# Kernel optimization log

Hardware: AMD Instinct MI355X
Metric: run time of the kernel (lower is better)

Reference implementation:

```python
import jax, jax.numpy as jnp
import numpy as np
from jax import lax

BS, CNT, W, P, E, K, L = 32, 128, 2048, 1024, 8, 25, 2


def setup_inputs() -> dict:
    key = jax.random.key(0)
    ks = jax.random.split(key, 12)
    s = lambda k, shape, scale: jax.random.normal(k, shape, dtype=jnp.float32) * scale
    return {
        "x": s(ks[0], (BS, CNT, W), 1.0),
        "conv_w": s(ks[1], (L, E, 1, K), 0.2),
        "conv_b": s(ks[2], (L, E), 0.02),
        "wq": s(ks[3], (L, P, W), 0.02),
        "bq": s(ks[4], (L, P), 0.02),
        "wk": s(ks[5], (L, P, W), 0.02),
        "bk": s(ks[6], (L, P), 0.02),
        "wv": s(ks[7], (L, P, W), 0.02),
        "bv": s(ks[8], (L, P), 0.02),
        "wo": s(ks[9], (L, W, P), 0.02),
        "bo": s(ks[10], (L, W), 0.02),
    }


def _moe(x, w, b):
    # x: [bs, cnt, W]; w: [E, 1, K]; b: [E]
    bs, cnt, d = x.shape
    xf = x.reshape(bs * cnt, 1, d)
    pad = K // 2
    y = lax.conv_general_dilated(
        xf, w, window_strides=(1,), padding=[(pad, pad)],
        dimension_numbers=("NCH", "OIH", "NCH"))  # [bs*cnt, E, W]
    y = y + b[None, :, None]
    return y.mean(axis=1).reshape(bs, cnt, d)


def _fe(x, wq, bq, wk, bk, wv, bv, wo, bo):
    # x: [bs, cnt, W]; projections to P, FFT-domain attention, back to W
    q = jnp.einsum("bcw,pw->bcp", x, wq) + bq
    k = jnp.einsum("bcw,pw->bcp", x, wk) + bk
    v = jnp.einsum("bcw,pw->bcp", x, wv) + bv
    q_fft = jnp.fft.fft(q, axis=-1)
    k_fft = jnp.fft.fft(k, axis=-1)
    v_fft = jnp.fft.fft(v, axis=-1)
    scale = jnp.sqrt(jnp.float32(P))
    weighted = (k_fft * jnp.conj(q_fft)) / scale * v_fft
    wv_real = jnp.fft.ifft(weighted, axis=-1).real.astype(x.dtype)
    return jnp.einsum("bcp,wp->bcw", wv_real, wo) + bo


def reference(x, conv_w, conv_b, wq, bq, wk, bk, wv, bv, wo, bo):
    for l in range(L):
        x = _moe(x, conv_w[l], conv_b[l])
        x = _fe(x, wq[l], bq[l], wk[l], bk[l], wv[l], bv[l], wo[l], bo[l])
    return x
```

## Files before the change

### kernel.cpp

```cpp
#include <hip/hip_runtime.h>
#include <hip/hip_bf16.h>

#define BSZ 32
#define CNTS 128
#define WD 2048
#define PD 1024
#define ED 8
#define KSZ 25
#define LN 2
#define MROWS (BSZ*CNTS)
#define QKVN (3*PD)
#define NWL (PD*WD)

typedef _Float16 f16;
typedef __attribute__((ext_vector_type(8))) _Float16 f16x8;
typedef __attribute__((ext_vector_type(4))) float f32x4;
typedef __attribute__((ext_vector_type(2))) float f32x2;

#define PI_F 3.14159265358979323846f

__global__ __launch_bounds__(256) void cvt_layer(
    const float* __restrict__ wq, const float* __restrict__ wk,
    const float* __restrict__ wv, const float* __restrict__ wo,
    f16* __restrict__ wqkv16, f16* __restrict__ wo16)
{
    const int i = (blockIdx.x * 256 + threadIdx.x) * 4;
    const float* src;
    f16* dst;
    if (i < 3*NWL) {
        dst = wqkv16 + i;
        src = (i < NWL) ? wq + i : (i < 2*NWL) ? wk + (i - NWL) : wv + (i - 2*NWL);
    } else {
        dst = wo16 + (i - 3*NWL);
        src = wo + (i - 3*NWL);
    }
    const float4 v = *(const float4*)src;
    f16 o[4];
    o[0] = (f16)v.x; o[1] = (f16)v.y; o[2] = (f16)v.z; o[3] = (f16)v.w;
    *(ushort4*)dst = *(const ushort4*)o;
}

template<typename IT>
__global__ __launch_bounds__(256) void conv_moe(
    const IT* __restrict__ xin,
    const float* __restrict__ cw,
    const float* __restrict__ cb,
    f16* __restrict__ xo)
{
    __shared__ float srow[WD];
    __shared__ float swb[KSZ];
    __shared__ float sbb;
    const int tid = threadIdx.x;
    const size_t row = blockIdx.x;
    if (tid < KSZ) {
        float s = 0.f;
        for (int e = 0; e < ED; ++e) s += cw[e*KSZ + tid];
        swb[tid] = s * (1.f/ED);
    }
    if (tid == 32) {
        float s = 0.f;
        for (int e = 0; e < ED; ++e) s += cb[e];
        sbb = s * (1.f/ED);
    }
    const IT* xr = xin + row*WD;
    if constexpr (sizeof(IT) == 2) {
        const f16x8 v = *(const f16x8*)(xr + tid*8);
        #pragma unroll
        for (int j = 0; j < 8; ++j) srow[tid*8 + j] = (float)v[j];
    } else {
        const float4 v0 = *(const float4*)(xr + tid*8);
        const float4 v1 = *(const float4*)(xr + tid*8 + 4);
        srow[tid*8+0] = v0.x; srow[tid*8+1] = v0.y; srow[tid*8+2] = v0.z; srow[tid*8+3] = v0.w;
        srow[tid*8+4] = v1.x; srow[tid*8+5] = v1.y; srow[tid*8+6] = v1.z; srow[tid*8+7] = v1.w;
    }
    __syncthreads();
    const float bb = sbb;
    float w[32];
    #pragma unroll
    for (int k = 0; k < 32; ++k) {
        const int idx = tid*8 + k - (KSZ/2);
        w[k] = (idx >= 0 && idx < WD) ? srow[idx] : 0.f;
    }
    f16 o[8];
    #pragma unroll
    for (int j = 0; j < 8; ++j) {
        float acc = bb;
        #pragma unroll
        for (int k = 0; k < KSZ; ++k) acc = fmaf(w[j+k], swb[k], acc);
        o[j] = (f16)acc;
    }
    *(f16x8*)(xo + row*WD + tid*8) = *(const f16x8*)o;
}

__global__ __launch_bounds__(512, 2) void gemm192(
    const f16* __restrict__ A,
    const f16* __restrict__ B,
    const float* __restrict__ c0, const float* __restrict__ c1, const float* __restrict__ c2,
    f16* __restrict__ out,
    const int K, const int N)
{
    __shared__ __align__(16) f16 sA[2][2][128*64];
    __shared__ __align__(16) f16 sB[2][3][64*64];

    const int tid  = threadIdx.x;
    const int lane = tid & 63;
    const int wave = tid >> 6;
    const int wr   = wave >> 2;
    const int wc   = wave & 3;
    const int quad = lane >> 4;
    const int r16  = lane & 15;
    const int xrA  = r16 & 7;

    const int orig = blockIdx.x;
    const int xcd  = orig & 7;
    const int loc  = orig >> 3;
    const int mt   = (xcd >> 1) * 4 + (loc & 3);
    const int nt   = (xcd & 1) * 8 + (loc >> 2);
    const int m0   = mt * 256;
    const int n0   = nt * 192;

    f32x4 acc[8][3] = {};
    f16x8 bf[3][2];
    f16x8 aX0, aX1, aX2, aX3, aY0, aY1, aY2, aY3, aZ0, aZ1, aZ2, aZ3;

    int soffA[2];
    #pragma unroll
    for (int t = 0; t < 2; ++t) {
        const int s = tid + 512*t;
        const int row = s >> 3;
        soffA[t] = row * K + (((s & 7) ^ (row & 7)) * 8);
    }
    int soffB;
    {
        const int row = tid >> 3;
        soffB = row * K + (((tid & 7) ^ (row & 7)) * 8);
    }

    int bPiece[3], bBase[3], bXor[3];
    #pragma unroll
    for (int j = 0; j < 3; ++j) {
        const int rb = wc*48 + j*16 + r16;
        bPiece[j] = rb >> 6;
        bBase[j]  = (rb & 63) << 3;
        bXor[j]   = rb & 7;
    }

    const f16* Abase[2] = { A + (size_t)m0 * K, A + (size_t)(m0 + 128) * K };
    const f16* Bp[3]    = { B + (size_t)n0 * K, B + (size_t)(n0 + 64) * K,
                            B + (size_t)(n0 + 128) * K };

    #define STAGE_A(BUF, HALF, GOFF)                                              \
      { _Pragma("unroll") for (int t = 0; t < 2; ++t) {                           \
          __builtin_amdgcn_global_load_lds(                                       \
            (const __attribute__((address_space(1))) unsigned int*)(Abase[HALF] + soffA[t] + (GOFF)), \
            (__attribute__((address_space(3))) unsigned int*)&sA[BUF][HALF][(tid + 512*t)*8], \
            16, 0, 0); } }

    #define STAGE_B(BUF, PIECE, GOFF)                                             \
      { __builtin_amdgcn_global_load_lds(                                         \
          (const __attribute__((address_space(1))) unsigned int*)(Bp[PIECE] + soffB + (GOFF)), \
          (__attribute__((address_space(3))) unsigned int*)&sB[BUF][PIECE][tid*8], \
          16, 0, 0); }

    #define LDA(BUF, ROW, C) \
      (*(const f16x8*)&sA[BUF][wr][ (((ROW) << 3) + ((C) ^ xrA)) * 8 ])

    #define LDB(BUF, J, C) \
      (*(const f16x8*)&sB[BUF][bPiece[J]][ (bBase[J] + ((C) ^ bXor[J])) * 8 ])

    #define READ_BF(BUF)                                                          \
      { _Pragma("unroll") for (int j = 0; j < 3; ++j) {                           \
          bf[j][0] = LDB(BUF, j, quad);                                           \
          bf[j][1] = LDB(BUF, j, 4 + quad);                                       \
        } }

    #define READ_A(BUF, Q, D0, D1, D2, D3)                                        \
      D0 = LDA(BUF, (2*(Q))*16   + r16, quad);                                    \
      D1 = LDA(BUF, (2*(Q))*16   + r16, 4 + quad);                                \
      D2 = LDA(BUF, (2*(Q)+1)*16 + r16, quad);                                    \
      D3 = LDA(BUF, (2*(Q)+1)*16 + r16, 4 + quad);

    #define MFMA_Q(Q, D0, D1, D2, D3)                                             \
      __builtin_amdgcn_s_setprio(1);                                              \
      { _Pragma("unroll") for (int jj = 0; jj < 3; ++jj) {                        \
          acc[2*(Q)][jj]   = __builtin_amdgcn_mfma_f32_16x16x32_f16(D0, bf[jj][0], acc[2*(Q)][jj],   0,0,0); \
          acc[2*(Q)+1][jj] = __builtin_amdgcn_mfma_f32_16x16x32_f16(D2, bf[jj][0], acc[2*(Q)+1][jj], 0,0,0); \
        } }                                                                       \
      { _Pragma("unroll") for (int jj = 0; jj < 3; ++jj) {                        \
          acc[2*(Q)][jj]   = __builtin_amdgcn_mfma_f32_16x16x32_f16(D1, bf[jj][1], acc[2*(Q)][jj],   0,0,0); \
          acc[2*(Q)+1][jj] = __builtin_amdgcn_mfma_f32_16x16x32_f16(D3, bf[jj][1], acc[2*(Q)+1][jj], 0,0,0); \
        } }                                                                       \
      __builtin_amdgcn_s_setprio(0);

    #define LGKM(n) asm volatile("s_waitcnt lgkmcnt(" #n ")" ::: "memory");       \
                    __builtin_amdgcn_sched_barrier(0);
    #define VMC(n)  asm volatile("s_waitcnt vmcnt(" #n ")" ::: "memory");
    #define BAR()   __builtin_amdgcn_s_barrier();

    STAGE_B(0, 0, 0); STAGE_B(0, 1, 0); STAGE_B(0, 2, 0);
    STAGE_A(0, 0, 0); STAGE_A(0, 1, 0);
    STAGE_B(1, 0, 64); STAGE_B(1, 1, 64); STAGE_B(1, 2, 64);
    VMC(3)
    BAR()

    const int NIT = K >> 7;
    for (int it = 0; it < NIT; ++it) {
        const bool kl = (it == NIT - 1);
        const int kb1 = (2*it + 1) * 64;
        const int kb2 = kb1 + 64;
        const int kb3 = kb1 + 128;

        STAGE_A(1, 0, kb1);
        READ_BF(0)
        READ_A(0, 0, aX0, aX1, aX2, aX3)
        LGKM(0)
        MFMA_Q(0, aX0, aX1, aX2, aX3)
        BAR()
        STAGE_A(1, 1, kb1);
        READ_A(0, 1, aY0, aY1, aY2, aY3)
        READ_A(0, 2, aZ0, aZ1, aZ2, aZ3)
        LGKM(4)
        MFMA_Q(1, aY0, aY1, aY2, aY3)
        if (!kl) { STAGE_B(0, 0, kb2); STAGE_B(0, 1, kb2); }
        READ_A(0, 3, aX0, aX1, aX2, aX3)
        LGKM(4)
        MFMA_Q(2, aZ0, aZ1, aZ2, aZ3)
        if (!kl) { STAGE_B(0, 2, kb2); }
        LGKM(0)
        MFMA_Q(3, aX0, aX1, aX2, aX3)
        if (!kl) { VMC(3) } else { VMC(0) }
        BAR()

        if (!kl) STAGE_A(0, 0, kb2);
        READ_BF(1)
        READ_A(1, 0, aX0, aX1, aX2, aX3)
        LGKM(0)
        MFMA_Q(0, aX0, aX1, aX2, aX3)
        BAR()
        if (!kl) STAGE_A(0, 1, kb2);
        READ_A(1, 1, aY0, aY1, aY2, aY3)
        READ_A(1, 2, aZ0, aZ1, aZ2, aZ3)
        LGKM(4)
        MFMA_Q(1, aY0, aY1, aY2, aY3)
        if (!kl) { STAGE_B(1, 0, kb3); STAGE_B(1, 1, kb3); }
        READ_A(1, 3, aX0, aX1, aX2, aX3)
        LGKM(4)
        MFMA_Q(2, aZ0, aZ1, aZ2, aZ3)
        if (!kl) { STAGE_B(1, 2, kb3); }
        LGKM(0)
        MFMA_Q(3, aX0, aX1, aX2, aX3)
        if (!kl) { VMC(3) }
        BAR()
    }

    #pragma unroll
    for (int j = 0; j < 3; ++j) {
        const int col = n0 + wc*48 + j*16 + r16;
        const float bv = (col < 1024) ? c0[col] : (col < 2048) ? c1[col-1024] : c2[col-2048];
        #pragma unroll
        for (int mi = 0; mi < 8; ++mi) {
            #pragma unroll
            for (int r = 0; r < 4; ++r) {
                const int rowg = m0 + wr*128 + mi*16 + quad*4 + r;
                out[(size_t)rowg*N + col] = (f16)(acc[mi][j][r] + bv);
            }
        }
    }

    #undef STAGE_A
    #undef STAGE_B
    #undef LDA
    #undef LDB
    #undef READ_BF
    #undef READ_A
    #undef MFMA_Q
    #undef LGKM
    #undef VMC
    #undef BAR
}

template<typename OT>
__global__ __launch_bounds__(512, 2) void gemmOP(
    const f16* __restrict__ A,
    const f16* __restrict__ B,
    const float* __restrict__ c0, const float* __restrict__ c1,
    OT* __restrict__ out,
    const int K, const int N)
{
    __shared__ __align__(16) f16 sA[2][2][128*64];
    __shared__ __align__(16) f16 sB[2][2][64*64];

    const int tid  = threadIdx.x;
    const int lane = tid & 63;
    const int wave = tid >> 6;
    const int wr   = wave >> 2;
    const int wc   = wave & 3;
    const int quad = lane >> 4;
    const int r16  = lane & 15;
    const int xrA  = r16 & 7;

    const int orig = blockIdx.x;
    const int xcd  = orig & 7;
    const int loc  = orig >> 3;
    const int mt   = (xcd >> 1) * 4 + (loc & 3);
    const int nt   = (xcd & 1) * 8 + (loc >> 2);
    const int m0   = mt * 256;
    const int n0   = nt * 128;

    f32x4 acc[8][2] = {};
    f16x8 bf[2][2];
    f16x8 aX0, aX1, aX2, aX3, aY0, aY1, aY2, aY3, aZ0, aZ1, aZ2, aZ3;

    int soffA[2];
    #pragma unroll
    for (int t = 0; t < 2; ++t) {
        const int s = tid + 512*t;
        const int row = s >> 3;
        soffA[t] = row * K + (((s & 7) ^ (row & 7)) * 8);
    }
    int soffB;
    {
        const int row = tid >> 3;
        soffB = row * K + (((tid & 7) ^ (row & 7)) * 8);
    }

    int bPiece[2], bBase[2], bXor[2];
    #pragma unroll
    for (int j = 0; j < 2; ++j) {
        const int rb = wc*32 + j*16 + r16;
        bPiece[j] = rb >> 6;
        bBase[j]  = (rb & 63) << 3;
        bXor[j]   = rb & 7;
    }

    const f16* Abase[2] = { A + (size_t)m0 * K, A + (size_t)(m0 + 128) * K };
    const f16* Bp[2]    = { B + (size_t)n0 * K, B + (size_t)(n0 + 64) * K };

    #define STAGE_A(BUF, HALF, GOFF)                                              \
      { _Pragma("unroll") for (int t = 0; t < 2; ++t) {                           \
          __builtin_amdgcn_global_load_lds(                                       \
            (const __attribute__((address_space(1))) unsigned int*)(Abase[HALF] + soffA[t] + (GOFF)), \
            (__attribute__((address_space(3))) unsigned int*)&sA[BUF][HALF][(tid + 512*t)*8], \
            16, 0, 0); } }

    #define STAGE_B(BUF, PIECE, GOFF)                                             \
      { __builtin_amdgcn_global_load_lds(                                         \
          (const __attribute__((address_space(1))) unsigned int*)(Bp[PIECE] + soffB + (GOFF)), \
          (__attribute__((address_space(3))) unsigned int*)&sB[BUF][PIECE][tid*8], \
          16, 0, 0); }

    #define LDA(BUF, ROW, C) \
      (*(const f16x8*)&sA[BUF][wr][ (((ROW) << 3) + ((C) ^ xrA)) * 8 ])

    #define LDB(BUF, J, C) \
      (*(const f16x8*)&sB[BUF][bPiece[J]][ (bBase[J] + ((C) ^ bXor[J])) * 8 ])

    #define READ_BF(BUF)                                                          \
      { _Pragma("unroll") for (int j = 0; j < 2; ++j) {                           \
          bf[j][0] = LDB(BUF, j, quad);                                           \
          bf[j][1] = LDB(BUF, j, 4 + quad);                                       \
        } }

    #define READ_A(BUF, Q, D0, D1, D2, D3)                                        \
      D0 = LDA(BUF, (2*(Q))*16   + r16, quad);                                    \
      D1 = LDA(BUF, (2*(Q))*16   + r16, 4 + quad);                                \
      D2 = LDA(BUF, (2*(Q)+1)*16 + r16, quad);                                    \
      D3 = LDA(BUF, (2*(Q)+1)*16 + r16, 4 + quad);

    #define MFMA_Q(Q, D0, D1, D2, D3)                                             \
      __builtin_amdgcn_s_setprio(1);                                              \
      { _Pragma("unroll") for (int jj = 0; jj < 2; ++jj) {                        \
          acc[2*(Q)][jj]   = __builtin_amdgcn_mfma_f32_16x16x32_f16(D0, bf[jj][0], acc[2*(Q)][jj],   0,0,0); \
          acc[2*(Q)+1][jj] = __builtin_amdgcn_mfma_f32_16x16x32_f16(D2, bf[jj][0], acc[2*(Q)+1][jj], 0,0,0); \
        } }                                                                       \
      { _Pragma("unroll") for (int jj = 0; jj < 2; ++jj) {                        \
          acc[2*(Q)][jj]   = __builtin_amdgcn_mfma_f32_16x16x32_f16(D1, bf[jj][1], acc[2*(Q)][jj],   0,0,0); \
          acc[2*(Q)+1][jj] = __builtin_amdgcn_mfma_f32_16x16x32_f16(D3, bf[jj][1], acc[2*(Q)+1][jj], 0,0,0); \
        } }                                                                       \
      __builtin_amdgcn_s_setprio(0);

    #define LGKM(n) asm volatile("s_waitcnt lgkmcnt(" #n ")" ::: "memory");       \
                    __builtin_amdgcn_sched_barrier(0);
    #define VMC(n)  asm volatile("s_waitcnt vmcnt(" #n ")" ::: "memory");
    #define BAR()   __builtin_amdgcn_s_barrier();

    STAGE_B(0, 0, 0); STAGE_B(0, 1, 0);
    STAGE_A(0, 0, 0); STAGE_A(0, 1, 0);
    STAGE_B(1, 0, 64); STAGE_B(1, 1, 64);
    VMC(2)
    BAR()

    const int NIT = K >> 7;
    for (int it = 0; it < NIT; ++it) {
        const bool kl = (it == NIT - 1);
        const int kb1 = (2*it + 1) * 64;
        const int kb2 = kb1 + 64;
        const int kb3 = kb1 + 128;

        STAGE_A(1, 0, kb1);
        READ_BF(0)
        READ_A(0, 0, aX0, aX1, aX2, aX3)
        LGKM(0)
        MFMA_Q(0, aX0, aX1, aX2, aX3)
        BAR()
        STAGE_A(1, 1, kb1);
        READ_A(0, 1, aY0, aY1, aY2, aY3)
        READ_A(0, 2, aZ0, aZ1, aZ2, aZ3)
        LGKM(4)
        MFMA_Q(1, aY0, aY1, aY2, aY3)
        if (!kl) { STAGE_B(0, 0, kb2); }
        READ_A(0, 3, aX0, aX1, aX2, aX3)
        LGKM(4)
        MFMA_Q(2, aZ0, aZ1, aZ2, aZ3)
        if (!kl) { STAGE_B(0, 1, kb2); }
        LGKM(0)
        MFMA_Q(3, aX0, aX1, aX2, aX3)
        if (!kl) { VMC(2) } else { VMC(0) }
        BAR()

        if (!kl) STAGE_A(0, 0, kb2);
        READ_BF(1)
        READ_A(1, 0, aX0, aX1, aX2, aX3)
        LGKM(0)
        MFMA_Q(0, aX0, aX1, aX2, aX3)
        BAR()
        if (!kl) STAGE_A(0, 1, kb2);
        READ_A(1, 1, aY0, aY1, aY2, aY3)
        READ_A(1, 2, aZ0, aZ1, aZ2, aZ3)
        LGKM(4)
        MFMA_Q(1, aY0, aY1, aY2, aY3)
        if (!kl) { STAGE_B(1, 0, kb3); }
        READ_A(1, 3, aX0, aX1, aX2, aX3)
        LGKM(4)
        MFMA_Q(2, aZ0, aZ1, aZ2, aZ3)
        if (!kl) { STAGE_B(1, 1, kb3); }
        LGKM(0)
        MFMA_Q(3, aX0, aX1, aX2, aX3)
        if (!kl) { VMC(2) }
        BAR()
    }

    #pragma unroll
    for (int j = 0; j < 2; ++j) {
        const int col = n0 + wc*32 + j*16 + r16;
        const float bv = (col < 1024) ? c0[col] : c1[col-1024];
        #pragma unroll
        for (int mi = 0; mi < 8; ++mi) {
            #pragma unroll
            for (int r = 0; r < 4; ++r) {
                const int rowg = m0 + wr*128 + mi*16 + quad*4 + r;
                out[(size_t)rowg*N + col] = (OT)(acc[mi][j][r] + bv);
            }
        }
    }

    #undef STAGE_A
    #undef STAGE_B
    #undef LDA
    #undef LDB
    #undef READ_BF
    #undef READ_A
    #undef MFMA_Q
    #undef LGKM
    #undef VMC
    #undef BAR
}

__device__ __forceinline__ f32x2 cmul2(const f32x2 a, const float wc, const float ws) {
    f32x2 r; r.x = a.x*wc - a.y*ws; r.y = a.y*wc + a.x*ws; return r;
}

#define IZ(c,i) ((c)*65 + ((i) ^ ((((i) >> 4) & 3) << 2)))
#define WSYNC() { asm volatile("s_waitcnt lgkmcnt(0)" ::: "memory"); \
                  __builtin_amdgcn_sched_barrier(0); }

__global__ __launch_bounds__(256) void fft_attn_wave(
    const f16* __restrict__ qkv, f16* __restrict__ outg)
{
    __shared__ f32x2 ZZ[4][2][16*65];
    const int tid = threadIdx.x;
    const int w   = tid >> 6;
    const int l   = tid & 63;
    const int t   = l & 15;
    const int cg  = l >> 4;
    f32x2* Z1 = &ZZ[w][0][0];
    f32x2* Z2 = &ZZ[w][1][0];
    f16*   sc = (f16*)Z1;

    const size_t rp = (size_t)blockIdx.x*4 + w;
    const f16* r1 = qkv + (2*rp)*QKVN;
    const f16* r2 = r1 + QKVN;

    float bwc[16], bws[16];
    {
        const float th = -2.f*PI_F*(float)l*(1.f/1024.f);
        bwc[0]=1.f; bws[0]=0.f;
        __sincosf(th,     &bws[1], &bwc[1]);
        __sincosf(2.f*th, &bws[2], &bwc[2]);
        __sincosf(4.f*th, &bws[4], &bwc[4]);
        __sincosf(8.f*th, &bws[8], &bwc[8]);
        bwc[3]=bwc[1]*bwc[2]-bws[1]*bws[2]; bws[3]=bws[1]*bwc[2]+bwc[1]*bws[2];
        bwc[5]=bwc[1]*bwc[4]-bws[1]*bws[4]; bws[5]=bws[1]*bwc[4]+bwc[1]*bws[4];
        bwc[6]=bwc[2]*bwc[4]-bws[2]*bws[4]; bws[6]=bws[2]*bwc[4]+bwc[2]*bws[4];
        bwc[7]=bwc[3]*bwc[4]-bws[3]*bws[4]; bws[7]=bws[3]*bwc[4]+bwc[3]*bws[4];
        #pragma unroll
        for (int k = 9; k < 16; ++k) {
            bwc[k]=bwc[k-8]*bwc[8]-bws[k-8]*bws[8];
            bws[k]=bws[k-8]*bwc[8]+bwc[k-8]*bws[8];
        }
    }
    float c0s, c0c, c1s, c1c;
    __sincosf(-2.f*PI_F*(float)t*(1.f/64.f), &c0s, &c0c);
    __sincosf(-2.f*PI_F*(float)(t>>2)*(1.f/16.f), &c1s, &c1c);

    const float W16C[10] = {1.f, 0.92387953f, 0.70710678f, 0.38268343f, 0.f,
                            0.f, -0.70710678f, 0.f, 0.f, -0.92387953f};
    const float W16S[10] = {0.f, -0.38268343f, -0.70710678f, -0.92387953f, -1.f,
                            0.f, -0.70710678f, 0.f, 0.f, 0.38268343f};

    f32x2 v[16], V1[16], V2[16];

    auto run_fft = [&]() {
        f32x2 C[4][4];
        #pragma unroll
        for (int jj = 0; jj < 4; ++jj) {
            const f32x2 a = v[jj], b = v[jj+4], c = v[jj+8], d = v[jj+12];
            f32x2 t0, t1, t2, t3;
            t0.x=a.x+c.x; t0.y=a.y+c.y; t1.x=a.x-c.x; t1.y=a.y-c.y;
            t2.x=b.x+d.x; t2.y=b.y+d.y; t3.x=b.x-d.x; t3.y=b.y-d.y;
            f32x2 B0, B1, B2, B3;
            B0.x=t0.x+t2.x; B0.y=t0.y+t2.y;
            B1.x=t1.x+t3.y; B1.y=t1.y-t3.x;
            B2.x=t0.x-t2.x; B2.y=t0.y-t2.y;
            B3.x=t1.x-t3.y; B3.y=t1.y+t3.x;
            C[0][jj] = B0;
            C[1][jj] = cmul2(B1, W16C[jj],   W16S[jj]);
            C[2][jj] = cmul2(B2, W16C[2*jj], W16S[2*jj]);
            C[3][jj] = cmul2(B3, W16C[3*jj], W16S[3*jj]);
        }
        f32x2 g[16];
        #pragma unroll
        for (int q = 0; q < 4; ++q) {
            const f32x2 c0 = C[q][0], c1 = C[q][1], c2 = C[q][2], c3 = C[q][3];
            f32x2 e0, o0, e1, o1;
            e0.x=c0.x+c2.x; e0.y=c0.y+c2.y; o0.x=c1.x+c3.x; o0.y=c1.y+c3.y;
            e1.x=c0.x-c2.x; e1.y=c0.y-c2.y; o1.x=c1.x-c3.x; o1.y=c1.y-c3.y;
            g[q].x    = e0.x+o0.x; g[q].y    = e0.y+o0.y;
            g[q+4].x  = e1.x+o1.y; g[q+4].y  = e1.y-o1.x;
            g[q+8].x  = e0.x-o0.x; g[q+8].y  = e0.y-o0.y;
            g[q+12].x = e1.x-o1.y; g[q+12].y = e1.y+o1.x;
        }
        WSYNC()
        #pragma unroll
        for (int k = 0; k < 16; ++k)
            Z1[IZ(k, l)] = cmul2(g[k], bwc[k], bws[k]);
        WSYNC()
        #pragma unroll
        for (int pass = 0; pass < 4; ++pass) {
            const int c = cg + 4*pass;
            const f32x2 a = Z1[IZ(c, t)],     b = Z1[IZ(c, t+16)];
            const f32x2 cc = Z1[IZ(c, t+32)], d = Z1[IZ(c, t+48)];
            const float apcx=a.x+cc.x, apcy=a.y+cc.y, amcx=a.x-cc.x, amcy=a.y-cc.y;
            const float bpdx=b.x+d.x,  bpdy=b.y+d.y,  bmdx=b.x-d.x,  bmdy=b.y-d.y;
            f32x2 y0; y0.x=apcx+bpdx; y0.y=apcy+bpdy;
            const float t1x=amcx+bmdy, t1y=amcy-bmdx;
            const float t2x=apcx-bpdx, t2y=apcy-bpdy;
            const float t3x=amcx-bmdy, t3y=amcy+bmdx;
            const float w2x=c0c*c0c-c0s*c0s, w2y=2.f*c0c*c0s;
            const float w3x=w2x*c0c-w2y*c0s, w3y=w2x*c0s+w2y*c0c;
            f32x2 y1; y1.x=c0c*t1x-c0s*t1y; y1.y=c0c*t1y+c0s*t1x;
            f32x2 y2; y2.x=w2x*t2x-w2y*t2y; y2.y=w2x*t2y+w2y*t2x;
            f32x2 y3; y3.x=w3x*t3x-w3y*t3y; y3.y=w3x*t3y+w3y*t3x;
            const int i0 = 4*t;
            Z2[IZ(c, i0)]   = y0; Z2[IZ(c, i0+1)] = y1;
            Z2[IZ(c, i0+2)] = y2; Z2[IZ(c, i0+3)] = y3;
        }
        WSYNC()
        #pragma unroll
        for (int pass = 0; pass < 4; ++pass) {
            const int c = cg + 4*pass;
            const f32x2 a = Z2[IZ(c, t)],     b = Z2[IZ(c, t+16)];
            const f32x2 cc = Z2[IZ(c, t+32)], d = Z2[IZ(c, t+48)];
            const float apcx=a.x+cc.x, apcy=a.y+cc.y, amcx=a.x-cc.x, amcy=a.y-cc.y;
            const float bpdx=b.x+d.x,  bpdy=b.y+d.y,  bmdx=b.x-d.x,  bmdy=b.y-d.y;
            f32x2 y0; y0.x=apcx+bpdx; y0.y=apcy+bpdy;
            const float t1x=amcx+bmdy, t1y=amcy-bmdx;
            const float t2x=apcx-bpdx, t2y=apcy-bpdy;
            const float t3x=amcx-bmdy, t3y=amcy+bmdx;
            const float w2x=c1c*c1c-c1s*c1s, w2y=2.f*c1c*c1s;
            const float w3x=w2x*c1c-w2y*c1s, w3y=w2x*c1s+w2y*c1c;
            f32x2 y1; y1.x=c1c*t1x-c1s*t1y; y1.y=c1c*t1y+c1s*t1x;
            f32x2 y2; y2.x=w2x*t2x-w2y*t2y; y2.y=w2x*t2y+w2y*t2x;
            f32x2 y3; y3.x=w3x*t3x-w3y*t3y; y3.y=w3x*t3y+w3y*t3x;
            const int i0 = (t & 3) + 16*(t >> 2);
            Z1[IZ(c, i0)]    = y0; Z1[IZ(c, i0+4)]  = y1;
            Z1[IZ(c, i0+8)]  = y2; Z1[IZ(c, i0+12)] = y3;
        }
        WSYNC()
        #pragma unroll
        for (int pass = 0; pass < 4; ++pass) {
            const int c = cg + 4*pass;
            const f32x2 a = Z1[IZ(c, t)],     b = Z1[IZ(c, t+16)];
            const f32x2 cc = Z1[IZ(c, t+32)], d = Z1[IZ(c, t+48)];
            const float apcx=a.x+cc.x, apcy=a.y+cc.y, amcx=a.x-cc.x, amcy=a.y-cc.y;
            const float bpdx=b.x+d.x,  bpdy=b.y+d.y,  bmdx=b.x-d.x,  bmdy=b.y-d.y;
            f32x2 y0; y0.x=apcx+bpdx; y0.y=apcy+bpdy;
            f32x2 y1; y1.x=amcx+bmdy; y1.y=amcy-bmdx;
            f32x2 y2; y2.x=apcx-bpdx; y2.y=apcy-bpdy;
            f32x2 y3; y3.x=amcx-bmdy; y3.y=amcy+bmdx;
            Z2[IZ(c, t)]    = y0; Z2[IZ(c, t+16)] = y1;
            Z2[IZ(c, t+32)] = y2; Z2[IZ(c, t+48)] = y3;
        }
        WSYNC()
    };

    auto stage2 = [&](const f16* a, const f16* b) {
        const f16x8 a0 = *(const f16x8*)(a + l*8);
        const f16x8 a1 = *(const f16x8*)(a + (l+64)*8);
        const f16x8 b0 = *(const f16x8*)(b + l*8);
        const f16x8 b1 = *(const f16x8*)(b + (l+64)*8);
        WSYNC()
        *(f16x8*)&sc[l*8]          = a0;
        *(f16x8*)&sc[(l+64)*8]     = a1;
        *(f16x8*)&sc[1024+l*8]     = b0;
        *(f16x8*)&sc[1024+(l+64)*8]= b1;
        WSYNC()
    };

    stage2(r1 + 2048, r2 + 2048);
    #pragma unroll
    for (int j = 0; j < 16; ++j) {
        v[j].x = (float)sc[l + 64*j];
        v[j].y = (float)sc[1024 + l + 64*j];
    }
    run_fft();
    #pragma unroll
    for (int j = 0; j < 16; ++j) {
        const int f = l + 64*j;
        const int gg = (PD - f) & (PD-1);
        const f32x2 z1 = Z2[IZ(f & 15, f >> 4)];
        const f32x2 z2 = Z2[IZ(gg & 15, gg >> 4)];
        V1[j].x = 0.5f*(z1.x + z2.x); V1[j].y = 0.5f*(z1.y - z2.y);
        V2[j].x = 0.5f*(z1.y + z2.y); V2[j].y = 0.5f*(z2.x - z1.x);
    }

    {
        const f16x8 a0 = *(const f16x8*)(r1 + l*8);
        const f16x8 a1 = *(const f16x8*)(r1 + (l+64)*8);
        const f16x8 a2 = *(const f16x8*)(r1 + (l+128)*8);
        const f16x8 a3 = *(const f16x8*)(r1 + (l+192)*8);
        WSYNC()
        *(f16x8*)&sc[l*8]        = a0;
        *(f16x8*)&sc[(l+64)*8]   = a1;
        *(f16x8*)&sc[(l+128)*8]  = a2;
        *(f16x8*)&sc[(l+192)*8]  = a3;
        WSYNC()
    }
    #pragma unroll
    for (int j = 0; j < 16; ++j) {
        v[j].x = (float)sc[l + 64*j];
        v[j].y = (float)sc[1024 + l + 64*j];
    }
    run_fft();
    #pragma unroll
    for (int j = 0; j < 16; ++j) {
        const int f = l + 64*j;
        const int gg = (PD - f) & (PD-1);
        const f32x2 z1 = Z2[IZ(f & 15, f >> 4)];
        const f32x2 z2 = Z2[IZ(gg & 15, gg >> 4)];
        const float Qr = 0.5f*(z1.x + z2.x), Qi = 0.5f*(z1.y - z2.y);
        const float Kr = 0.5f*(z1.y + z2.y), Ki = 0.5f*(z2.x - z1.x);
        const float Pr = (Kr*Qr + Ki*Qi) * (1.f/32.f);
        const float Pi = (Ki*Qr - Kr*Qi) * (1.f/32.f);
        const float sx = Pr*V1[j].x - Pi*V1[j].y;
        const float sy = -(Pr*V1[j].y + Pi*V1[j].x);
        V1[j].x = sx; V1[j].y = sy;
    }

    {
        const f16x8 a0 = *(const f16x8*)(r2 + l*8);
        const f16x8 a1 = *(const f16x8*)(r2 + (l+64)*8);
        const f16x8 a2 = *(const f16x8*)(r2 + (l+128)*8);
        const f16x8 a3 = *(const f16x8*)(r2 + (l+192)*8);
        WSYNC()
        *(f16x8*)&sc[l*8]        = a0;
        *(f16x8*)&sc[(l+64)*8]   = a1;
        *(f16x8*)&sc[(l+128)*8]  = a2;
        *(f16x8*)&sc[(l+192)*8]  = a3;
        WSYNC()
    }
    #pragma unroll
    for (int j = 0; j < 16; ++j) {
        v[j].x = (float)sc[l + 64*j];
        v[j].y = (float)sc[1024 + l + 64*j];
    }
    run_fft();
    #pragma unroll
    for (int j = 0; j < 16; ++j) {
        const int f = l + 64*j;
        const int gg = (PD - f) & (PD-1);
        const f32x2 z1 = Z2[IZ(f & 15, f >> 4)];
        const f32x2 z2 = Z2[IZ(gg & 15, gg >> 4)];
        const float Qr = 0.5f*(z1.x + z2.x), Qi = 0.5f*(z1.y - z2.y);
        const float Kr = 0.5f*(z1.y + z2.y), Ki = 0.5f*(z2.x - z1.x);
        const float Pr = (Kr*Qr + Ki*Qi) * (1.f/32.f);
        const float Pi = (Ki*Qr - Kr*Qi) * (1.f/32.f);
        const float sx = Pr*V2[j].x - Pi*V2[j].y;
        const float sy = -(Pr*V2[j].y + Pi*V2[j].x);
        V2[j].x = sx; V2[j].y = sy;
    }

    #pragma unroll
    for (int j = 0; j < 16; ++j) {
        v[j].x = V1[j].x - V2[j].y;
        v[j].y = V1[j].y + V2[j].x;
    }
    run_fft();

    #pragma unroll
    for (int j = 0; j < 16; ++j) {
        const int n = l + 64*j;
        const f32x2 z = Z2[IZ(n & 15, n >> 4)];
        sc[n]        = (f16)(z.x * (1.f/1024.f));
        sc[1024 + n] = (f16)(z.y * (1.f/1024.f));
    }
    WSYNC()
    f16* o1 = outg + (2*rp)*PD;
    f16* o2 = o1 + PD;
    *(f16x8*)(o1 + l*8)      = *(const f16x8*)&sc[l*8];
    *(f16x8*)(o1 + (l+64)*8) = *(const f16x8*)&sc[(l+64)*8];
    *(f16x8*)(o2 + l*8)      = *(const f16x8*)&sc[1024 + l*8];
    *(f16x8*)(o2 + (l+64)*8) = *(const f16x8*)&sc[1024 + (l+64)*8];
}

extern "C" void kernel_launch(void* const* d_in, const int* in_sizes, int n_in,
                              void* d_out, int out_size, void* d_ws, size_t ws_size,
                              hipStream_t stream)
{
    const float* x      = (const float*)d_in[0];
    const float* conv_w = (const float*)d_in[1];
    const float* conv_b = (const float*)d_in[2];
    const float* wq     = (const float*)d_in[3];
    const float* bq     = (const float*)d_in[4];
    const float* wk     = (const float*)d_in[5];
    const float* bk     = (const float*)d_in[6];
    const float* wv     = (const float*)d_in[7];
    const float* bv     = (const float*)d_in[8];
    const float* wo     = (const float*)d_in[9];
    const float* bo     = (const float*)d_in[10];

    char* ws = (char*)d_ws;
    const size_t MB = 1024*1024;
    f16*   wqkv16 = (f16*)(ws);
    f16*   wo16   = (f16*)(ws + 12*MB);
    f16*   qkvbuf = (f16*)(ws + 16*MB);
    f16*   xc16   = (f16*)(ws + 40*MB);
    f16*   xmid   = (f16*)(ws + 56*MB);
    f16*   wvr16  = xc16;

    for (int l = 0; l < LN; ++l) {
        cvt_layer<<<dim3(4*NWL/4/256), dim3(256), 0, stream>>>(
            wq + (size_t)l*NWL, wk + (size_t)l*NWL, wv + (size_t)l*NWL, wo + (size_t)l*NWL,
            wqkv16, wo16);

        if (l == 0)
            conv_moe<float><<<dim3(MROWS), dim3(256), 0, stream>>>(
                x, conv_w, conv_b, xc16);
        else
            conv_moe<f16><<<dim3(MROWS), dim3(256), 0, stream>>>(
                xmid, conv_w + (size_t)l*ED*KSZ, conv_b + (size_t)l*ED, xc16);

        gemm192<<<dim3((MROWS/256)*(QKVN/192)), dim3(512), 0, stream>>>(
            xc16, wqkv16,
            bq + (size_t)l*PD, bk + (size_t)l*PD, bv + (size_t)l*PD,
            qkvbuf, WD, QKVN);

        fft_attn_wave<<<dim3(MROWS/8), dim3(256), 0, stream>>>(qkvbuf, wvr16);

        if (l == LN-1)
            gemmOP<float><<<dim3((MROWS/256)*(WD/128)), dim3(512), 0, stream>>>(
                wvr16, wo16,
                bo + (size_t)l*WD, bo + (size_t)l*WD + PD,
                (float*)d_out, PD, WD);
        else
            gemmOP<f16><<<dim3((MROWS/256)*(WD/128)), dim3(512), 0, stream>>>(
                wvr16, wo16,
                bo + (size_t)l*WD, bo + (size_t)l*WD + PD,
                xmid, PD, WD);
    }
}
```

Baseline: 427.0 us.

## Fuse per-layer kernels into persistent megakernel with grid barriers

Replaces the five per-layer launches (weight conversion, conv, QKV GEMM, FFT attention, output GEMM) with one persistent 256-block kernel per layer. The phases are separated by atomic-counter grid barriers and reuse one shared memory buffer. The goal is to remove launch gaps and tail effects between the small kernels. In exchange it forces one block per CU with a fixed grid, which can hurt occupancy in the GEMM and FFT phases. It also relies on all 256 blocks being co-resident for the barriers to avoid deadlock.

```diff
diff --git a/kernel.cpp b/kernel.cpp
--- a/kernel.cpp
+++ b/kernel.cpp
@@ -19,88 +19,40 @@
 
 #define PI_F 3.14159265358979323846f
 
-__global__ __launch_bounds__(256) void cvt_layer(
-    const float* __restrict__ wq, const float* __restrict__ wk,
-    const float* __restrict__ wv, const float* __restrict__ wo,
-    f16* __restrict__ wqkv16, f16* __restrict__ wo16)
+__device__ unsigned g_cnt[8];
+
+__device__ __forceinline__ void grid_barrier(int b)
 {
-    const int i = (blockIdx.x * 256 + threadIdx.x) * 4;
-    const float* src;
-    f16* dst;
-    if (i < 3*NWL) {
-        dst = wqkv16 + i;
-        src = (i < NWL) ? wq + i : (i < 2*NWL) ? wk + (i - NWL) : wv + (i - 2*NWL);
-    } else {
-        dst = wo16 + (i - 3*NWL);
-        src = wo + (i - 3*NWL);
-    }
-    const float4 v = *(const float4*)src;
-    f16 o[4];
-    o[0] = (f16)v.x; o[1] = (f16)v.y; o[2] = (f16)v.z; o[3] = (f16)v.w;
-    *(ushort4*)dst = *(const ushort4*)o;
+    __syncthreads();
+    if (threadIdx.x == 0) {
+        __threadfence();
+        const unsigned old = __hip_atomic_fetch_add(&g_cnt[b], 1u,
+                                __ATOMIC_ACQ_REL, __HIP_MEMORY_SCOPE_AGENT);
+        const unsigned target = (old & ~255u) + 256u;
+        while (__hip_atomic_load(&g_cnt[b],
+                   __ATOMIC_ACQUIRE, __HIP_MEMORY_SCOPE_AGENT) < target)
+            __builtin_amdgcn_s_sleep(2);
+    }
+    __syncthreads();
 }
 
-template<typename IT>
-__global__ __launch_bounds__(256) void conv_moe(
-    const IT* __restrict__ xin,
-    const float* __restrict__ cw,
-    const float* __restrict__ cb,
-    f16* __restrict__ xo)
+__device__ __forceinline__ f32x2 cmul2(const f32x2 a, const float wc, const float ws) {
+    f32x2 r; r.x = a.x*wc - a.y*ws; r.y = a.y*wc + a.x*ws; return r;
+}
+
+#define IZ(c,i) ((c)*65 + ((i) ^ ((((i) >> 4) & 3) << 2)))
+#define WSYNC() { asm volatile("s_waitcnt lgkmcnt(0)" ::: "memory"); \
+                  __builtin_amdgcn_sched_barrier(0); }
+
+__device__ __forceinline__ void gemm192_phase(
+    char* smem,
+    const f16* __restrict__ A, const f16* __restrict__ B,
+    const float* __restrict__ c0, const float* __restrict__ c1, const float* __restrict__ c2,
+    f16* __restrict__ out)
 {
-    __shared__ float srow[WD];
-    __shared__ float swb[KSZ];
-    __shared__ float sbb;
-    const int tid = threadIdx.x;
-    const size_t row = blockIdx.x;
-    if (tid < KSZ) {
-        float s = 0.f;
-        for (int e = 0; e < ED; ++e) s += cw[e*KSZ + tid];
-        swb[tid] = s * (1.f/ED);
-    }
-    if (tid == 32) {
-        float s = 0.f;
-        for (int e = 0; e < ED; ++e) s += cb[e];
-        sbb = s * (1.f/ED);
-    }
-    const IT* xr = xin + row*WD;
-    if constexpr (sizeof(IT) == 2) {
-        const f16x8 v = *(const f16x8*)(xr + tid*8);
-        #pragma unroll
-        for (int j = 0; j < 8; ++j) srow[tid*8 + j] = (float)v[j];
-    } else {
-        const float4 v0 = *(const float4*)(xr + tid*8);
-        const float4 v1 = *(const float4*)(xr + tid*8 + 4);
-        srow[tid*8+0] = v0.x; srow[tid*8+1] = v0.y; srow[tid*8+2] = v0.z; srow[tid*8+3] = v0.w;
-        srow[tid*8+4] = v1.x; srow[tid*8+5] = v1.y; srow[tid*8+6] = v1.z; srow[tid*8+7] = v1.w;
-    }
-    __syncthreads();
-    const float bb = sbb;
-    float w[32];
-    #pragma unroll
-    for (int k = 0; k < 32; ++k) {
-        const int idx = tid*8 + k - (KSZ/2);
-        w[k] = (idx >= 0 && idx < WD) ? srow[idx] : 0.f;
-    }
-    f16 o[8];
-    #pragma unroll
-    for (int j = 0; j < 8; ++j) {
-        float acc = bb;
-        #pragma unroll
-        for (int k = 0; k < KSZ; ++k) acc = fmaf(w[j+k], swb[k], acc);
-        o[j] = (f16)acc;
-    }
-    *(f16x8*)(xo + row*WD + tid*8) = *(const f16x8*)o;
-}
-
-__global__ __launch_bounds__(512, 2) void gemm192(
-    const f16* __restrict__ A,
-    const f16* __restrict__ B,
-    const float* __restrict__ c0, const float* __restrict__ c1, const float* __restrict__ c2,
-    f16* __restrict__ out,
-    const int K, const int N)
-{
-    __shared__ __align__(16) f16 sA[2][2][128*64];
-    __shared__ __align__(16) f16 sB[2][3][64*64];
+    const int K = WD, N = QKVN;
+    f16* sAb = (f16*)smem;
+    f16* sBb = (f16*)(smem + 65536);
 
     const int tid  = threadIdx.x;
     const int lane = tid & 63;
@@ -149,24 +101,27 @@
     const f16* Bp[3]    = { B + (size_t)n0 * K, B + (size_t)(n0 + 64) * K,
                             B + (size_t)(n0 + 128) * K };
 
+    #define G1_SA(BUF,HALF) (sAb + ((BUF)*2 + (HALF)) * 8192)
+    #define G1_SB(BUF,PIECE) (sBb + ((BUF)*3 + (PIECE)) * 4096)
+
     #define STAGE_A(BUF, HALF, GOFF)                                              \
       { _Pragma("unroll") for (int t = 0; t < 2; ++t) {                           \
           __builtin_amdgcn_global_load_lds(                                       \
             (const __attribute__((address_space(1))) unsigned int*)(Abase[HALF] + soffA[t] + (GOFF)), \
-            (__attribute__((address_space(3))) unsigned int*)&sA[BUF][HALF][(tid + 512*t)*8], \
+            (__attribute__((address_space(3))) unsigned int*)(G1_SA(BUF,HALF) + (tid + 512*t)*8), \
             16, 0, 0); } }
 
     #define STAGE_B(BUF, PIECE, GOFF)                                             \
       { __builtin_amdgcn_global_load_lds(                                         \
           (const __attribute__((address_space(1))) unsigned int*)(Bp[PIECE] + soffB + (GOFF)), \
-          (__attribute__((address_space(3))) unsigned int*)&sB[BUF][PIECE][tid*8], \
+          (__attribute__((address_space(3))) unsigned int*)(G1_SB(BUF,PIECE) + tid*8), \
           16, 0, 0); }
 
     #define LDA(BUF, ROW, C) \
-      (*(const f16x8*)&sA[BUF][wr][ (((ROW) << 3) + ((C) ^ xrA)) * 8 ])
+      (*(const f16x8*)(G1_SA(BUF,wr) + ((((ROW) << 3) + ((C) ^ xrA)) * 8)))
 
     #define LDB(BUF, J, C) \
-      (*(const f16x8*)&sB[BUF][bPiece[J]][ (bBase[J] + ((C) ^ bXor[J])) * 8 ])
+      (*(const f16x8*)(G1_SB(BUF,bPiece[J]) + ((bBase[J] + ((C) ^ bXor[J])) * 8)))
 
     #define READ_BF(BUF)                                                          \
       { _Pragma("unroll") for (int j = 0; j < 3; ++j) {                           \
@@ -267,6 +222,8 @@
         }
     }
 
+    #undef G1_SA
+    #undef G1_SB
     #undef STAGE_A
     #undef STAGE_B
     #undef LDA
@@ -280,15 +237,15 @@
 }
 
 template<typename OT>
-__global__ __launch_bounds__(512, 2) void gemmOP(
-    const f16* __restrict__ A,
-    const f16* __restrict__ B,
+__device__ __forceinline__ void gemmOP_phase(
+    char* smem,
+    const f16* __restrict__ A, const f16* __restrict__ B,
     const float* __restrict__ c0, const float* __restrict__ c1,
-    OT* __restrict__ out,
-    const int K, const int N)
+    OT* __restrict__ out)
 {
-    __shared__ __align__(16) f16 sA[2][2][128*64];
-    __shared__ __align__(16) f16 sB[2][2][64*64];
+    const int K = PD, N = WD;
+    f16* sAb = (f16*)smem;
+    f16* sBb = (f16*)(smem + 65536);
 
     const int tid  = threadIdx.x;
     const int lane = tid & 63;
@@ -336,24 +293,27 @@
     const f16* Abase[2] = { A + (size_t)m0 * K, A + (size_t)(m0 + 128) * K };
     const f16* Bp[2]    = { B + (size_t)n0 * K, B + (size_t)(n0 + 64) * K };
 
+    #define G3_SA(BUF,HALF) (sAb + ((BUF)*2 + (HALF)) * 8192)
+    #define G3_SB(BUF,PIECE) (sBb + ((BUF)*2 + (PIECE)) * 4096)
+
     #define STAGE_A(BUF, HALF, GOFF)                                              \
       { _Pragma("unroll") for (int t = 0; t < 2; ++t) {                           \
           __builtin_amdgcn_global_load_lds(                                       \
             (const __attribute__((address_space(1))) unsigned int*)(Abase[HALF] + soffA[t] + (GOFF)), \
-            (__attribute__((address_space(3))) unsigned int*)&sA[BUF][HALF][(tid + 512*t)*8], \
+            (__attribute__((address_space(3))) unsigned int*)(G3_SA(BUF,HALF) + (tid + 512*t)*8), \
             16, 0, 0); } }
 
     #define STAGE_B(BUF, PIECE, GOFF)                                             \
       { __builtin_amdgcn_global_load_lds(                                         \
           (const __attribute__((address_space(1))) unsigned int*)(Bp[PIECE] + soffB + (GOFF)), \
-          (__attribute__((address_space(3))) unsigned int*)&sB[BUF][PIECE][tid*8], \
+          (__attribute__((address_space(3))) unsigned int*)(G3_SB(BUF,PIECE) + tid*8), \
           16, 0, 0); }
 
     #define LDA(BUF, ROW, C) \
-      (*(const f16x8*)&sA[BUF][wr][ (((ROW) << 3) + ((C) ^ xrA)) * 8 ])
+      (*(const f16x8*)(G3_SA(BUF,wr) + ((((ROW) << 3) + ((C) ^ xrA)) * 8)))
 
     #define LDB(BUF, J, C) \
-      (*(const f16x8*)&sB[BUF][bPiece[J]][ (bBase[J] + ((C) ^ bXor[J])) * 8 ])
+      (*(const f16x8*)(G3_SB(BUF,bPiece[J]) + ((bBase[J] + ((C) ^ bXor[J])) * 8)))
 
     #define READ_BF(BUF)                                                          \
       { _Pragma("unroll") for (int j = 0; j < 2; ++j) {                           \
@@ -454,6 +414,8 @@
         }
     }
 
+    #undef G3_SA
+    #undef G3_SB
     #undef STAGE_A
     #undef STAGE_B
     #undef LDA
@@ -466,28 +428,19 @@
     #undef BAR
 }
 
-__device__ __forceinline__ f32x2 cmul2(const f32x2 a, const float wc, const float ws) {
-    f32x2 r; r.x = a.x*wc - a.y*ws; r.y = a.y*wc + a.x*ws; return r;
-}
-
-#define IZ(c,i) ((c)*65 + ((i) ^ ((((i) >> 4) & 3) << 2)))
-#define WSYNC() { asm volatile("s_waitcnt lgkmcnt(0)" ::: "memory"); \
-                  __builtin_amdgcn_sched_barrier(0); }
-
-__global__ __launch_bounds__(256) void fft_attn_wave(
-    const f16* __restrict__ qkv, f16* __restrict__ outg)
+__device__ __forceinline__ void attn_phase(
+    char* smem, const f16* __restrict__ qkv, f16* __restrict__ outg)
 {
-    __shared__ f32x2 ZZ[4][2][16*65];
     const int tid = threadIdx.x;
     const int w   = tid >> 6;
     const int l   = tid & 63;
     const int t   = l & 15;
     const int cg  = l >> 4;
-    f32x2* Z1 = &ZZ[w][0][0];
-    f32x2* Z2 = &ZZ[w][1][0];
+    f32x2* Z1 = (f32x2*)smem + (size_t)w * 2080;
+    f32x2* Z2 = Z1 + 1040;
     f16*   sc = (f16*)Z1;
 
-    const size_t rp = (size_t)blockIdx.x*4 + w;
+    const size_t rp = (size_t)blockIdx.x*8 + w;
     const f16* r1 = qkv + (2*rp)*QKVN;
     const f16* r2 = r1 + QKVN;
 
@@ -614,7 +567,7 @@
         WSYNC()
     };
 
-    auto stage2 = [&](const f16* a, const f16* b) {
+    auto load16 = [&](const f16* a, const f16* b) {
         const f16x8 a0 = *(const f16x8*)(a + l*8);
         const f16x8 a1 = *(const f16x8*)(a + (l+64)*8);
         const f16x8 b0 = *(const f16x8*)(b + l*8);
@@ -625,14 +578,14 @@
         *(f16x8*)&sc[1024+l*8]     = b0;
         *(f16x8*)&sc[1024+(l+64)*8]= b1;
         WSYNC()
+        #pragma unroll
+        for (int j = 0; j < 16; ++j) {
+            v[j].x = (float)sc[l + 64*j];
+            v[j].y = (float)sc[1024 + l + 64*j];
+        }
     };
 
-    stage2(r1 + 2048, r2 + 2048);
-    #pragma unroll
-    for (int j = 0; j < 16; ++j) {
-        v[j].x = (float)sc[l + 64*j];
-        v[j].y = (float)sc[1024 + l + 64*j];
-    }
+    load16(r1 + 2048, r2 + 2048);
     run_fft();
     #pragma unroll
     for (int j = 0; j < 16; ++j) {
@@ -644,23 +597,7 @@
         V2[j].x = 0.5f*(z1.y + z2.y); V2[j].y = 0.5f*(z2.x - z1.x);
     }
 
-    {
-        const f16x8 a0 = *(const f16x8*)(r1 + l*8);
-        const f16x8 a1 = *(const f16x8*)(r1 + (l+64)*8);
-        const f16x8 a2 = *(const f16x8*)(r1 + (l+128)*8);
-        const f16x8 a3 = *(const f16x8*)(r1 + (l+192)*8);
-        WSYNC()
-        *(f16x8*)&sc[l*8]        = a0;
-        *(f16x8*)&sc[(l+64)*8]   = a1;
-        *(f16x8*)&sc[(l+128)*8]  = a2;
-        *(f16x8*)&sc[(l+192)*8]  = a3;
-        WSYNC()
-    }
-    #pragma unroll
-    for (int j = 0; j < 16; ++j) {
-        v[j].x = (float)sc[l + 64*j];
-        v[j].y = (float)sc[1024 + l + 64*j];
-    }
+    load16(r1, r1 + 1024);
     run_fft();
     #pragma unroll
     for (int j = 0; j < 16; ++j) {
@@ -677,23 +614,7 @@
         V1[j].x = sx; V1[j].y = sy;
     }
 
-    {
-        const f16x8 a0 = *(const f16x8*)(r2 + l*8);
-        const f16x8 a1 = *(const f16x8*)(r2 + (l+64)*8);
-        const f16x8 a2 = *(const f16x8*)(r2 + (l+128)*8);
-        const f16x8 a3 = *(const f16x8*)(r2 + (l+192)*8);
-        WSYNC()
-        *(f16x8*)&sc[l*8]        = a0;
-        *(f16x8*)&sc[(l+64)*8]   = a1;
-        *(f16x8*)&sc[(l+128)*8]  = a2;
-        *(f16x8*)&sc[(l+192)*8]  = a3;
-        WSYNC()
-    }
-    #pragma unroll
-    for (int j = 0; j < 16; ++j) {
-        v[j].x = (float)sc[l + 64*j];
-        v[j].y = (float)sc[1024 + l + 64*j];
-    }
+    load16(r2, r2 + 1024);
     run_fft();
     #pragma unroll
     for (int j = 0; j < 16; ++j) {
@@ -731,6 +652,101 @@
     *(f16x8*)(o1 + (l+64)*8) = *(const f16x8*)&sc[(l+64)*8];
     *(f16x8*)(o2 + l*8)      = *(const f16x8*)&sc[1024 + l*8];
     *(f16x8*)(o2 + (l+64)*8) = *(const f16x8*)&sc[1024 + (l+64)*8];
+}
+
+template<typename IT, typename OT>
+__global__ __launch_bounds__(512, 1) void layer_mega(
+    const IT* __restrict__ xin,
+    const float* __restrict__ cw, const float* __restrict__ cb,
+    const float* __restrict__ wq, const float* __restrict__ wk,
+    const float* __restrict__ wv, const float* __restrict__ wo,
+    const float* __restrict__ bq, const float* __restrict__ bk,
+    const float* __restrict__ bv, const float* __restrict__ bo,
+    f16* wqkv16, f16* wo16, f16* qkvbuf, f16* xc16, f16* wvr16,
+    OT* __restrict__ xout,
+    const int bbase)
+{
+    __shared__ __align__(16) char smem[133120];
+    const int tid = threadIdx.x;
+
+    {
+        const int g = blockIdx.x*512 + tid;
+        for (int it = 0; it < 16; ++it) {
+            const int i = (g + 131072*it) * 4;
+            const float* src; f16* dst;
+            if (i < 3*NWL) {
+                dst = wqkv16 + i;
+                src = (i < NWL) ? wq + i : (i < 2*NWL) ? wk + (i - NWL) : wv + (i - 2*NWL);
+            } else {
+                dst = wo16 + (i - 3*NWL);
+                src = wo + (i - 3*NWL);
+            }
+            const float4 v4 = *(const float4*)src;
+            f16 o[4];
+            o[0]=(f16)v4.x; o[1]=(f16)v4.y; o[2]=(f16)v4.z; o[3]=(f16)v4.w;
+            *(ushort4*)dst = *(const ushort4*)o;
+        }
+
+        float* srow = (float*)smem;
+        float* swb  = (float*)(smem + 16384);
+        float* sbb  = (float*)(smem + 16484);
+        if (tid < KSZ) {
+            float s = 0.f;
+            for (int e = 0; e < ED; ++e) s += cw[e*KSZ + tid];
+            swb[tid] = s * (1.f/ED);
+        }
+        if (tid == 32) {
+            float s = 0.f;
+            for (int e = 0; e < ED; ++e) s += cb[e];
+            *sbb = s * (1.f/ED);
+        }
+        __syncthreads();
+        const float bb = *sbb;
+        const int r  = tid >> 8;
+        const int t8 = tid & 255;
+        for (int p = 0; p < 8; ++p) {
+            const size_t row = (size_t)blockIdx.x*16 + p*2 + r;
+            const IT* xr = xin + row*WD;
+            if constexpr (sizeof(IT) == 2) {
+                const f16x8 v8 = *(const f16x8*)(xr + t8*8);
+                #pragma unroll
+                for (int j = 0; j < 8; ++j) srow[r*2048 + t8*8 + j] = (float)v8[j];
+            } else {
+                const float4 v0 = *(const float4*)(xr + t8*8);
+                const float4 v1 = *(const float4*)(xr + t8*8 + 4);
+                srow[r*2048+t8*8+0]=v0.x; srow[r*2048+t8*8+1]=v0.y;
+                srow[r*2048+t8*8+2]=v0.z; srow[r*2048+t8*8+3]=v0.w;
+                srow[r*2048+t8*8+4]=v1.x; srow[r*2048+t8*8+5]=v1.y;
+                srow[r*2048+t8*8+6]=v1.z; srow[r*2048+t8*8+7]=v1.w;
+            }
+            __syncthreads();
+            float wv_[32];
+            #pragma unroll
+            for (int k = 0; k < 32; ++k) {
+                const int idx = t8*8 + k - (KSZ/2);
+                wv_[k] = (idx >= 0 && idx < WD) ? srow[r*2048 + idx] : 0.f;
+            }
+            f16 o[8];
+            #pragma unroll
+            for (int j = 0; j < 8; ++j) {
+                float acc = bb;
+                #pragma unroll
+                for (int k = 0; k < KSZ; ++k) acc = fmaf(wv_[j+k], swb[k], acc);
+                o[j] = (f16)acc;
+            }
+            *(f16x8*)(xc16 + row*WD + t8*8) = *(const f16x8*)o;
+            __syncthreads();
+        }
+    }
+    grid_barrier(bbase + 0);
+
+    gemm192_phase(smem, xc16, wqkv16, bq, bk, bv, qkvbuf);
+    grid_barrier(bbase + 1);
+
+    attn_phase(smem, qkvbuf, wvr16);
+    grid_barrier(bbase + 2);
+
+    gemmOP_phase<OT>(smem, wvr16, wo16, bo, bo + PD, xout);
 }
 
 extern "C" void kernel_launch(void* const* d_in, const int* in_sizes, int n_in,
@@ -758,34 +774,14 @@
     f16*   xmid   = (f16*)(ws + 56*MB);
     f16*   wvr16  = xc16;
 
-    for (int l = 0; l < LN; ++l) {
-        cvt_layer<<<dim3(4*NWL/4/256), dim3(256), 0, stream>>>(
-            wq + (size_t)l*NWL, wk + (size_t)l*NWL, wv + (size_t)l*NWL, wo + (size_t)l*NWL,
-            wqkv16, wo16);
-
-        if (l == 0)
-            conv_moe<float><<<dim3(MROWS), dim3(256), 0, stream>>>(
-                x, conv_w, conv_b, xc16);
-        else
-            conv_moe<f16><<<dim3(MROWS), dim3(256), 0, stream>>>(
-                xmid, conv_w + (size_t)l*ED*KSZ, conv_b + (size_t)l*ED, xc16);
-
-        gemm192<<<dim3((MROWS/256)*(QKVN/192)), dim3(512), 0, stream>>>(
-            xc16, wqkv16,
-            bq + (size_t)l*PD, bk + (size_t)l*PD, bv + (size_t)l*PD,
-            qkvbuf, WD, QKVN);
-
-        fft_attn_wave<<<dim3(MROWS/8), dim3(256), 0, stream>>>(qkvbuf, wvr16);
-
-        if (l == LN-1)
-            gemmOP<float><<<dim3((MROWS/256)*(WD/128)), dim3(512), 0, stream>>>(
-                wvr16, wo16,
-                bo + (size_t)l*WD, bo + (size_t)l*WD + PD,
-                (float*)d_out, PD, WD);
-        else
-            gemmOP<f16><<<dim3((MROWS/256)*(WD/128)), dim3(512), 0, stream>>>(
-                wvr16, wo16,
-                bo + (size_t)l*WD, bo + (size_t)l*WD + PD,
-                xmid, PD, WD);
-    }
+    layer_mega<float, f16><<<dim3(256), dim3(512), 0, stream>>>(
+        x, conv_w, conv_b,
+        wq, wk, wv, wo, bq, bk, bv, bo,
+        wqkv16, wo16, qkvbuf, xc16, wvr16, xmid, 0);
+
+    layer_mega<f16, float><<<dim3(256), dim3(512), 0, stream>>>(
+        xmid, conv_w + (size_t)ED*KSZ, conv_b + ED,
+        wq + (size_t)NWL, wk + (size_t)NWL, wv + (size_t)NWL, wo + (size_t)NWL,
+        bq + PD, bk + PD, bv + PD, bo + WD,
+        wqkv16, wo16, qkvbuf, xc16, wvr16, (float*)d_out, 3);
 }
```

Measured after the change: 694.4 us. 1.63x slower.
